# Kernel tuning notes

Hardware: AMD Instinct MI355X
Metric: run time of the kernel (lower is better)

The kernel has to match this reference:

```python
import jax, jax.numpy as jnp
import numpy as np

B, K, H, W = 8, 1024, 24, 24
C = H * W            # in_channels = 576
NH = 6               # hardcoded num_heads
HD = C // NH         # 96


def setup_inputs() -> dict:
    key = jax.random.key(0)
    ks = jax.random.split(key, 8)
    s = 1.0 / np.sqrt(C)
    return {
        "input1": jax.random.normal(ks[0], (B, K, H, W), jnp.float32),
        "input2": jax.random.normal(ks[1], (B, K, H, W), jnp.float32),
        "Wq": jax.random.uniform(ks[2], (C, C), jnp.float32, -s, s),
        "bq": jax.random.uniform(ks[3], (C,), jnp.float32, -s, s),
        "Wk": jax.random.uniform(ks[4], (C, C), jnp.float32, -s, s),
        "bk": jax.random.uniform(ks[5], (C,), jnp.float32, -s, s),
        "Wv": jax.random.uniform(ks[6], (C, C), jnp.float32, -s, s),
        "bv": jax.random.uniform(ks[7], (C,), jnp.float32, -s, s),
    }


def reference(input1, input2, Wq, bq, Wk, bk, Wv, bv):
    b, k, h, w = input1.shape
    c = h * w
    x1 = input1.reshape(b, k, c)
    x2 = input2.reshape(b, k, c)
    # torch nn.Linear: y = x @ W^T + b
    q = x1 @ Wq.T + bq                      # [b, k, c]
    kk = x2 @ Wk.T + bk
    v = x2 @ Wv.T + bv
    # torch .view scrambles: [b, k, c] -> [b, NH, c//NH, k] (row-major reshape)
    q = q.reshape(b, NH, c // NH, k)
    kk = kk.reshape(b, NH, c // NH, k)
    v = v.reshape(b, NH, c // NH, k)
    # scores = q^T k over head-dim; NOTE: no 1/sqrt(d) scaling in original
    scores = jnp.einsum('bhdq,bhdk->bhqk', q, kk)   # [b, NH, k, k]
    weights = jax.nn.softmax(scores, axis=-1)
    # context = value @ weights^T -> [b, NH, hd, k]
    ctx = jnp.einsum('bhdk,bhqk->bhdq', v, weights)
    return ctx.reshape(b, k, h, w)
```

## Files before the change

kernel.cpp:

```cpp
#include <hip/hip_runtime.h>
#include <cmath>

#define BATCH 8
#define KDIM  1024
#define CH    576
#define NHEAD 6
#define HDIM  96

typedef _Float16 f16;
typedef f16 f16x4 __attribute__((ext_vector_type(4)));
typedef f16 f16x8 __attribute__((ext_vector_type(8)));
typedef float f32x16 __attribute__((ext_vector_type(16)));
typedef unsigned int u32;

#define PSZ  (BATCH * KDIM * CH)
#define WSZ  (CH * CH)

__device__ inline f32x16 zero16() {
    f32x16 z;
#pragma unroll
    for (int r = 0; r < 16; ++r) z[r] = 0.f;
    return z;
}

__global__ __launch_bounds__(256) void convert_kernel(
    const float* __restrict__ x1, const float* __restrict__ x2,
    const float* __restrict__ Wq, const float* __restrict__ Wk,
    const float* __restrict__ Wv,
    f16* __restrict__ x1h, f16* __restrict__ x2h, f16* __restrict__ wh)
{
    const int y = blockIdx.y;
    int idx = blockIdx.x * 256 + threadIdx.x;
    const float* src;
    f16* dst;
    if (y == 0) {
        if (idx >= PSZ / 8) return;
        src = x1; dst = x1h;
    } else if (y == 1) {
        if (idx >= PSZ / 8) return;
        src = x2; dst = x2h;
    } else {
        if (idx >= 3 * WSZ / 8) return;
        int seg = idx / (WSZ / 8);
        src = (seg == 0) ? Wq : (seg == 1) ? Wk : Wv;
        dst = wh + seg * WSZ;
        idx -= seg * (WSZ / 8);
    }
    float4 u0 = ((const float4*)src)[2 * idx];
    float4 u1 = ((const float4*)src)[2 * idx + 1];
    f16x8 hv;
    hv[0] = (f16)u0.x; hv[1] = (f16)u0.y; hv[2] = (f16)u0.z; hv[3] = (f16)u0.w;
    hv[4] = (f16)u1.x; hv[5] = (f16)u1.y; hv[6] = (f16)u1.z; hv[7] = (f16)u1.w;
    ((f16x8*)dst)[idx] = hv;
}

__global__ __launch_bounds__(256, 4) void proj_kernel(
    const f16* __restrict__ x1h, const f16* __restrict__ x2h,
    const f16* __restrict__ wh,
    const float* __restrict__ bq, const float* __restrict__ bk,
    const float* __restrict__ bv,
    f16* __restrict__ qf, f16* __restrict__ kf, f16* __restrict__ vf)
{
    const int z = blockIdx.z;
    const f16* A      = (z == 0) ? x1h : x2h;
    const f16* W      = wh + z * WSZ;
    const float* bias = (z == 0) ? bq : (z == 1) ? bk : bv;
    f16* dst          = (z == 0) ? qf : (z == 1) ? kf : vf;

    __shared__ f16 As[64 * 72];
    __shared__ f16 Ws[192 * 72];

    const int tid = threadIdx.x;
    const int lane = tid & 63, w = tid >> 6;
    const int l31 = lane & 31, half = lane >> 5;
    const int mw = 32 * (w & 1), nh = 96 * (w >> 1);
    const int nBase = blockIdx.x * 192;
    const int mBase = blockIdx.y * 64;

    int arow[2], ach[2], wrow[6], wch[6];
#pragma unroll
    for (int r = 0; r < 2; ++r) {
        int idx = r * 256 + tid;
        arow[r] = idx >> 3; ach[r] = idx & 7;
    }
#pragma unroll
    for (int r = 0; r < 6; ++r) {
        int idx = r * 256 + tid;
        wrow[r] = idx >> 3; wch[r] = idx & 7;
    }

    f16x8 aP[2], wP[6];
#pragma unroll
    for (int r = 0; r < 2; ++r)
        aP[r] = *(const f16x8*)&A[(size_t)(mBase + arow[r]) * CH + ach[r] * 8];
#pragma unroll
    for (int r = 0; r < 6; ++r)
        wP[r] = *(const f16x8*)&W[(size_t)(nBase + wrow[r]) * CH + wch[r] * 8];

    f32x16 acc[3] = {zero16(), zero16(), zero16()};

    for (int k0 = 0; k0 < CH; k0 += 64) {
        __syncthreads();
#pragma unroll
        for (int r = 0; r < 2; ++r)
            *(f16x8*)&As[arow[r] * 72 + ach[r] * 8] = aP[r];
#pragma unroll
        for (int r = 0; r < 6; ++r)
            *(f16x8*)&Ws[wrow[r] * 72 + wch[r] * 8] = wP[r];
        __syncthreads();
        if (k0 + 64 < CH) {
#pragma unroll
            for (int r = 0; r < 2; ++r)
                aP[r] = *(const f16x8*)&A[(size_t)(mBase + arow[r]) * CH + k0 + 64 + ach[r] * 8];
#pragma unroll
            for (int r = 0; r < 6; ++r)
                wP[r] = *(const f16x8*)&W[(size_t)(nBase + wrow[r]) * CH + k0 + 64 + wch[r] * 8];
        }
#pragma unroll
        for (int ks = 0; ks < 4; ++ks) {
            f16x8 a = *(const f16x8*)&As[(mw + l31) * 72 + 16 * ks + 8 * half];
#pragma unroll
            for (int nt = 0; nt < 3; ++nt) {
                f16x8 bfr = *(const f16x8*)&Ws[(nh + 32 * nt + l31) * 72 + 16 * ks + 8 * half];
                acc[nt] = __builtin_amdgcn_mfma_f32_32x32x16_f16(a, bfr, acc[nt], 0, 0, 0);
            }
        }
    }

#pragma unroll
    for (int nt = 0; nt < 3; ++nt) {
        int n = nBase + nh + 32 * nt + l31;
        float bsv = bias[n];
#pragma unroll
        for (int r = 0; r < 16; ++r) {
            int m = mBase + mw + (r & 3) + 8 * (r >> 2) + 4 * half;
            dst[(size_t)m * CH + n] = (f16)(acc[nt][r] + bsv);
        }
    }
}

__global__ __launch_bounds__(256) void transpose_qk(
    const f16* __restrict__ qf, const f16* __restrict__ kf,
    f16* __restrict__ QT, f16* __restrict__ KT)
{
    const int tt = blockIdx.x;
    const int bh = blockIdx.y;
    const f16* src = blockIdx.z ? kf : qf;
    f16* dst = blockIdx.z ? KT : QT;

    __shared__ f16 Ts[96 * 72];

    const int tid = threadIdx.x;
    const int rowbase = (bh / NHEAD) * CH + (bh % NHEAD) * HDIM;

#pragma unroll
    for (int r = 0; r < 3; ++r) {
        int idx = r * 256 + tid;
        int d = idx >> 3, g = idx & 7;
        *(f16x8*)&Ts[d * 72 + g * 8] =
            *(const f16x8*)&src[(size_t)(rowbase + d) * KDIM + tt * 64 + g * 8];
    }
    __syncthreads();
#pragma unroll
    for (int r = 0; r < 3; ++r) {
        int idx = r * 256 + tid;
        int t = idx & 63, dg = idx >> 6;
        f16x8 v;
#pragma unroll
        for (int u = 0; u < 8; ++u) v[u] = Ts[(dg * 8 + u) * 72 + t];
        *(f16x8*)&dst[((size_t)bh * KDIM + tt * 64 + t) * HDIM + dg * 8] = v;
    }
}

__global__ __launch_bounds__(256, 3) void attn_kernel(
    const f16* __restrict__ qT, const f16* __restrict__ kT,
    const f16* __restrict__ vf, float* __restrict__ out)
{
    __shared__ __align__(16) char smem[25600];

    const int bh = blockIdx.x;
    const int qt = blockIdx.y;
    const int h  = bh % NHEAD;
    const int b  = bh / NHEAD;

    const int tid = threadIdx.x;
    const int lane = tid & 63, w = tid >> 6;
    const int ih = w & 1, jg = w >> 1;
    const int l31 = lane & 31, half = lane >> 5;
    const int iw = 32 * ih;

    const f16* Qbase = qT + ((size_t)bh * KDIM + qt * 64) * HDIM;
    const f16* Kbase = kT + (size_t)bh * KDIM * HDIM;
    const f16* Vbase = vf + ((size_t)b * CH + (size_t)h * HDIM) * KDIM;

    f16x8 qfr[6];
#pragma unroll
    for (int ks = 0; ks < 6; ++ks) {
        qfr[ks] = *(const f16x8*)&Qbase[(size_t)(iw + l31) * HDIM + 16 * ks + 8 * half];
#pragma unroll
        for (int u = 0; u < 8; ++u)
            qfr[ks][u] = (f16)((float)qfr[ks][u] * 1.44269504f);
    }

    const f16* Kfrag = Kbase + (size_t)(32 * jg + l31) * HDIM + 8 * half;
    const f16* Vfrag = Vbase + (size_t)l31 * KDIM + 32 * jg + 8 * half;

    f16x8 kc[6], vc[6];
#pragma unroll
    for (int ks = 0; ks < 6; ++ks)
        kc[ks] = *(const f16x8*)&Kfrag[16 * ks];
#pragma unroll
    for (int kq = 0; kq < 2; ++kq)
#pragma unroll
        for (int t = 0; t < 3; ++t)
            vc[kq * 3 + t] = *(const f16x8*)&Vfrag[(size_t)(32 * t) * KDIM + 16 * kq];

    float l_run = 0.f;
    f32x16 Oacc[3] = {zero16(), zero16(), zero16()};

    for (int jt = 0; jt < KDIM; jt += 64) {
        f32x16 s0 = zero16();
#pragma unroll
        for (int ks = 0; ks < 6; ++ks)
            s0 = __builtin_amdgcn_mfma_f32_32x32x16_f16(kc[ks], qfr[ks], s0, 0, 0, 0);

        if (jt + 64 < KDIM) {
            const f16* Kt = Kfrag + (size_t)(jt + 64) * HDIM;
#pragma unroll
            for (int ks = 0; ks < 6; ++ks)
                kc[ks] = *(const f16x8*)&Kt[16 * ks];
        }

        f16x4 pq[4];
#pragma unroll
        for (int r = 0; r < 16; ++r) {
            float e = __builtin_amdgcn_exp2f(s0[r] - 26.0f);
            l_run += e;
            pq[r >> 2][r & 3] = (f16)e;
        }

#pragma unroll
        for (int kq = 0; kq < 2; ++kq) {
            union { f16x4 h; u32 u[2]; } snd, rcv, keep;
            keep.h = half ? pq[2 * kq + 1] : pq[2 * kq];
            snd.h  = half ? pq[2 * kq]     : pq[2 * kq + 1];
            rcv.u[0] = __shfl_xor((int)snd.u[0], 32);
            rcv.u[1] = __shfl_xor((int)snd.u[1], 32);
            f16x8 bp;
            if (half == 0) {
#pragma unroll
                for (int v = 0; v < 4; ++v) { bp[v] = keep.h[v]; bp[4 + v] = rcv.h[v]; }
            } else {
#pragma unroll
                for (int v = 0; v < 4; ++v) { bp[v] = rcv.h[v]; bp[4 + v] = keep.h[v]; }
            }
#pragma unroll
            for (int t = 0; t < 3; ++t)
                Oacc[t] = __builtin_amdgcn_mfma_f32_32x32x16_f16(vc[kq * 3 + t], bp, Oacc[t], 0, 0, 0);
        }

        if (jt + 64 < KDIM) {
            const f16* Vt = Vfrag + jt + 64;
#pragma unroll
            for (int kq = 0; kq < 2; ++kq)
#pragma unroll
                for (int t = 0; t < 3; ++t)
                    vc[kq * 3 + t] = *(const f16x8*)&Vt[(size_t)(32 * t) * KDIM + 16 * kq];
        }
    }

    l_run += __shfl_xor(l_run, 32);

    float* Oscr = (float*)smem;
    float* lScr = (float*)(smem + 25344);
    if (jg == 1) {
        if (half == 0) lScr[iw + l31] = l_run;
        float* od = Oscr + ih * 3168;
#pragma unroll
        for (int t = 0; t < 3; ++t)
#pragma unroll
            for (int r = 0; r < 16; ++r) {
                int d = 32 * t + (r & 3) + 8 * (r >> 2) + 4 * half;
                od[d * 33 + l31] = Oacc[t][r];
            }
    }
    __syncthreads();
    if (jg == 0) {
        float linv = 1.0f / (l_run + lScr[iw + l31]);
        const float* od = Oscr + ih * 3168;
        float* obase = out + ((size_t)b * CH + (size_t)h * HDIM) * KDIM
                           + qt * 64 + iw + l31;
#pragma unroll
        for (int t = 0; t < 3; ++t)
#pragma unroll
            for (int r = 0; r < 16; ++r) {
                int d = 32 * t + (r & 3) + 8 * (r >> 2) + 4 * half;
                obase[(size_t)d * KDIM] =
                    (Oacc[t][r] + od[d * 33 + l31]) * linv;
            }
    }
}

extern "C" void kernel_launch(void* const* d_in, const int* in_sizes, int n_in,
                              void* d_out, int out_size, void* d_ws, size_t ws_size,
                              hipStream_t stream)
{
    const float* x1 = (const float*)d_in[0];
    const float* x2 = (const float*)d_in[1];
    const float* Wq = (const float*)d_in[2];
    const float* bq = (const float*)d_in[3];
    const float* Wk = (const float*)d_in[4];
    const float* bk = (const float*)d_in[5];
    const float* Wv = (const float*)d_in[6];
    const float* bv = (const float*)d_in[7];
    float* out = (float*)d_out;

    const size_t P = PSZ;
    f16* x1h = (f16*)d_ws;
    f16* x2h = x1h + P;
    f16* qf  = x2h + P;
    f16* kf  = qf + P;
    f16* vf  = kf + P;
    f16* wh  = vf + P;
    f16* QT  = x1h;
    f16* KT  = x2h;

    dim3 cgrid((P / 8 + 255) / 256, 3);
    convert_kernel<<<cgrid, 256, 0, stream>>>(x1, x2, Wq, Wk, Wv, x1h, x2h, wh);

    dim3 pgrid(CH / 192, (BATCH * KDIM) / 64, 3);
    proj_kernel<<<pgrid, 256, 0, stream>>>(x1h, x2h, wh, bq, bk, bv, qf, kf, vf);

    dim3 tgrid(KDIM / 64, BATCH * NHEAD, 2);
    transpose_qk<<<tgrid, 256, 0, stream>>>(qf, kf, QT, KT);

    dim3 agrid(BATCH * NHEAD, KDIM / 64);
    attn_kernel<<<agrid, 256, 0, stream>>>(QT, KT, vf, out);
}
```

Baseline: 191.6 us.

## Repack Q, K, V into MFMA-fragment-ordered blocks for coalesced attention loads

Q and K are now repacked into per-64-token blocks laid out in the exact per-lane MFMA fragment order, and a new kernel does the same for V. The attention kernel's fragment loads thus become contiguous 16-byte-per-lane reads instead of strided rows. This targets uncoalesced global loads in the attention inner loop. It costs an extra launch and a full extra pass over V through memory.

```diff
diff --git a/kernel.cpp b/kernel.cpp
--- a/kernel.cpp
+++ b/kernel.cpp
@@ -139,14 +139,14 @@
     }
 }
 
-__global__ __launch_bounds__(256) void transpose_qk(
+__global__ __launch_bounds__(256) void repack_qk(
     const f16* __restrict__ qf, const f16* __restrict__ kf,
-    f16* __restrict__ QT, f16* __restrict__ KT)
+    f16* __restrict__ QF, f16* __restrict__ KF)
 {
     const int tt = blockIdx.x;
     const int bh = blockIdx.y;
     const f16* src = blockIdx.z ? kf : qf;
-    f16* dst = blockIdx.z ? KT : QT;
+    f16* dst = blockIdx.z ? KF : QF;
 
     __shared__ f16 Ts[96 * 72];
 
@@ -161,20 +161,52 @@
             *(const f16x8*)&src[(size_t)(rowbase + d) * KDIM + tt * 64 + g * 8];
     }
     __syncthreads();
+
+    f16* dblk = dst + ((size_t)bh * 16 + tt) * 6144;
 #pragma unroll
     for (int r = 0; r < 3; ++r) {
-        int idx = r * 256 + tid;
-        int t = idx & 63, dg = idx >> 6;
+        int c = r * 256 + tid;
+        int lane = c & 63;
+        int ks = (c >> 6) % 6;
+        int jg = c / 384;
+        int l31 = lane & 31, half = lane >> 5;
+        int jl = jg * 32 + l31;
+        int d0 = ks * 16 + half * 8;
         f16x8 v;
 #pragma unroll
-        for (int u = 0; u < 8; ++u) v[u] = Ts[(dg * 8 + u) * 72 + t];
-        *(f16x8*)&dst[((size_t)bh * KDIM + tt * 64 + t) * HDIM + dg * 8] = v;
+        for (int u = 0; u < 8; ++u) v[u] = Ts[(d0 + u) * 72 + jl];
+        *(f16x8*)&dblk[(size_t)c * 8] = v;
+    }
+}
+
+__global__ __launch_bounds__(256) void repack_v(
+    const f16* __restrict__ vf, f16* __restrict__ VF)
+{
+    const int tt = blockIdx.x;
+    const int bh = blockIdx.y;
+    const int tid = threadIdx.x;
+
+    const f16* vbase = vf + ((size_t)(bh / NHEAD) * CH + (bh % NHEAD) * HDIM) * KDIM;
+    f16* dblk = VF + ((size_t)bh * 16 + tt) * 6144;
+
+#pragma unroll
+    for (int r = 0; r < 3; ++r) {
+        int c = r * 256 + tid;
+        int lane = c & 63;
+        int t  = (c >> 6) % 3;
+        int kq = ((c >> 6) / 3) & 1;
+        int jg = c / 384;
+        int l31 = lane & 31, half = lane >> 5;
+        int d = t * 32 + l31;
+        int j = tt * 64 + jg * 32 + kq * 16 + half * 8;
+        f16x8 v = *(const f16x8*)&vbase[(size_t)d * KDIM + j];
+        *(f16x8*)&dblk[(size_t)c * 8] = v;
     }
 }
 
 __global__ __launch_bounds__(256, 3) void attn_kernel(
-    const f16* __restrict__ qT, const f16* __restrict__ kT,
-    const f16* __restrict__ vf, float* __restrict__ out)
+    const f16* __restrict__ QF, const f16* __restrict__ KF,
+    const f16* __restrict__ VF, float* __restrict__ out)
 {
     __shared__ __align__(16) char smem[25600];
 
@@ -189,46 +221,43 @@
     const int l31 = lane & 31, half = lane >> 5;
     const int iw = 32 * ih;
 
-    const f16* Qbase = qT + ((size_t)bh * KDIM + qt * 64) * HDIM;
-    const f16* Kbase = kT + (size_t)bh * KDIM * HDIM;
-    const f16* Vbase = vf + ((size_t)b * CH + (size_t)h * HDIM) * KDIM;
+    const f16* Qblk  = QF + ((size_t)bh * 16 + qt) * 6144 + (size_t)ih * 3072 + (size_t)lane * 8;
+    const f16* Kfrag = KF + (size_t)bh * 16 * 6144 + (size_t)jg * 3072 + (size_t)lane * 8;
+    const f16* Vfrag = VF + (size_t)bh * 16 * 6144 + (size_t)jg * 3072 + (size_t)lane * 8;
 
     f16x8 qfr[6];
 #pragma unroll
     for (int ks = 0; ks < 6; ++ks) {
-        qfr[ks] = *(const f16x8*)&Qbase[(size_t)(iw + l31) * HDIM + 16 * ks + 8 * half];
+        qfr[ks] = *(const f16x8*)&Qblk[ks * 512];
 #pragma unroll
         for (int u = 0; u < 8; ++u)
             qfr[ks][u] = (f16)((float)qfr[ks][u] * 1.44269504f);
     }
 
-    const f16* Kfrag = Kbase + (size_t)(32 * jg + l31) * HDIM + 8 * half;
-    const f16* Vfrag = Vbase + (size_t)l31 * KDIM + 32 * jg + 8 * half;
-
     f16x8 kc[6], vc[6];
 #pragma unroll
     for (int ks = 0; ks < 6; ++ks)
-        kc[ks] = *(const f16x8*)&Kfrag[16 * ks];
+        kc[ks] = *(const f16x8*)&Kfrag[ks * 512];
 #pragma unroll
     for (int kq = 0; kq < 2; ++kq)
 #pragma unroll
         for (int t = 0; t < 3; ++t)
-            vc[kq * 3 + t] = *(const f16x8*)&Vfrag[(size_t)(32 * t) * KDIM + 16 * kq];
+            vc[kq * 3 + t] = *(const f16x8*)&Vfrag[kq * 1536 + t * 512];
 
     float l_run = 0.f;
     f32x16 Oacc[3] = {zero16(), zero16(), zero16()};
 
-    for (int jt = 0; jt < KDIM; jt += 64) {
+    for (int jt = 0; jt < 16; ++jt) {
         f32x16 s0 = zero16();
 #pragma unroll
         for (int ks = 0; ks < 6; ++ks)
             s0 = __builtin_amdgcn_mfma_f32_32x32x16_f16(kc[ks], qfr[ks], s0, 0, 0, 0);
 
-        if (jt + 64 < KDIM) {
-            const f16* Kt = Kfrag + (size_t)(jt + 64) * HDIM;
+        if (jt + 1 < 16) {
+            const f16* Kt = Kfrag + (size_t)(jt + 1) * 6144;
 #pragma unroll
             for (int ks = 0; ks < 6; ++ks)
-                kc[ks] = *(const f16x8*)&Kt[16 * ks];
+                kc[ks] = *(const f16x8*)&Kt[ks * 512];
         }
 
         f16x4 pq[4];
@@ -259,13 +288,13 @@
                 Oacc[t] = __builtin_amdgcn_mfma_f32_32x32x16_f16(vc[kq * 3 + t], bp, Oacc[t], 0, 0, 0);
         }
 
-        if (jt + 64 < KDIM) {
-            const f16* Vt = Vfrag + jt + 64;
+        if (jt + 1 < 16) {
+            const f16* Vt = Vfrag + (size_t)(jt + 1) * 6144;
 #pragma unroll
             for (int kq = 0; kq < 2; ++kq)
 #pragma unroll
                 for (int t = 0; t < 3; ++t)
-                    vc[kq * 3 + t] = *(const f16x8*)&Vt[(size_t)(32 * t) * KDIM + 16 * kq];
+                    vc[kq * 3 + t] = *(const f16x8*)&Vt[kq * 1536 + t * 512];
         }
     }
 
@@ -322,8 +351,9 @@
     f16* kf  = qf + P;
     f16* vf  = kf + P;
     f16* wh  = vf + P;
-    f16* QT  = x1h;
-    f16* KT  = x2h;
+    f16* QF  = x1h;
+    f16* KF  = x2h;
+    f16* VF  = qf;
 
     dim3 cgrid((P / 8 + 255) / 256, 3);
     convert_kernel<<<cgrid, 256, 0, stream>>>(x1, x2, Wq, Wk, Wv, x1h, x2h, wh);
@@ -332,8 +362,11 @@
     proj_kernel<<<pgrid, 256, 0, stream>>>(x1h, x2h, wh, bq, bk, bv, qf, kf, vf);
 
     dim3 tgrid(KDIM / 64, BATCH * NHEAD, 2);
-    transpose_qk<<<tgrid, 256, 0, stream>>>(qf, kf, QT, KT);
+    repack_qk<<<tgrid, 256, 0, stream>>>(qf, kf, QF, KF);
+
+    dim3 vgrid(KDIM / 64, BATCH * NHEAD);
+    repack_v<<<vgrid, 256, 0, stream>>>(vf, VF);
 
     dim3 agrid(BATCH * NHEAD, KDIM / 64);
-    attn_kernel<<<agrid, 256, 0, stream>>>(QT, KT, vf, out);
-}
+    attn_kernel<<<agrid, 256, 0, stream>>>(QF, KF, VF, out);
+}
```

Measured after the change: 163.7 us. -14.5%, faster.
